# Kernel optimization log

Measured on AMD Instinct MI355X. Metric: run time of the kernel, lower is better.

## Reference

```python
import jax, jax.numpy as jnp
import numpy as np


def setup_inputs() -> dict:
    key = jax.random.key(0)
    B, L = 32, 512
    k1, k2, k3, k4 = jax.random.split(key, 4)
    acids = jax.random.normal(k1, (B, L), dtype=jnp.float32)
    mask = jnp.ones((B, L), dtype=jnp.float32)
    # Self-avoiding-style lattice walk: unit step along a random axis each move.
    axis = jax.random.randint(k3, (B, L - 1), 0, 3)
    sign = jax.random.randint(k4, (B, L - 1), 0, 2) * 2 - 1
    steps = (jax.nn.one_hot(axis, 3, dtype=jnp.int32) * sign[..., None]).astype(jnp.int32)
    idx = jnp.concatenate([jnp.zeros((B, 1, 3), jnp.int32), jnp.cumsum(steps, axis=1)], axis=1)
    idx = jnp.clip(idx, -(L - 1), L - 1)  # keep coords in the op's valid range
    return {"acids": acids, "mask": mask, "idx": idx, "protein_length": 512, "window_size": 9}


def reference(acids, mask, idx, protein_length, window_size):
    # acids: [B, L] float, mask: [B, L] float, idx: [B, L, 3] int lattice coords.
    L, W = protein_length, window_size
    B = acids.shape[0]
    W3 = W * W * W
    half = W // 2

    # Map walk coords [-(L-1), L-1] -> even grid coords [0, 4(L-1)].
    idx2 = 2 * (idx + (L - 1))                          # [B, L, 3] int32, all even
    # AVG pool window [2] stride 1 VALID on even ints -> exact integer midpoints.
    inter_idx = (idx2[:, :-1, :] + idx2[:, 1:, :]) // 2  # [B, L-1, 3] odd coords
    # 2 * avgpool(acids) + 1 == acids[i] + acids[i+1] + 1
    inter_vals = acids[:, :-1] + acids[:, 1:] + 1.0      # [B, L-1]

    cidx = jnp.concatenate([idx2, inter_idx], axis=1)    # [B, M, 3], M = 2L-1
    cval = jnp.concatenate([acids, inter_vals], axis=1)  # [B, M]
    cmask = jnp.concatenate([mask, mask[:, 1:]], axis=1) # [B, M]

    # Per residue i: a W^3 window centered at idx2[:, i]. Scatter every snake
    # point (residues + bond midpoints) that falls inside the window.
    rel = cidx[:, None, :, :] - idx2[:, :, None, :] + half     # [B, L, M, 3]
    valid = jnp.all((rel >= 0) & (rel < W), axis=-1)           # [B, L, M]
    lin = (rel[..., 0] * W + rel[..., 1]) * W + rel[..., 2]    # [B, L, M]
    lin = jnp.where(valid, lin, 0)
    val = jnp.where(valid, (cval * cmask)[:, None, :], 0.0)    # [B, L, M]

    b_off = jnp.arange(B, dtype=jnp.int32)[:, None, None] * (L * W3)
    i_off = jnp.arange(L, dtype=jnp.int32)[None, :, None] * W3
    g = (b_off + i_off + lin).reshape(-1)
    lattice = jnp.zeros((B * L * W3,), dtype=acids.dtype).at[g].add(val.reshape(-1))
    return lattice.reshape(B, L, W, W, W, 1)
```

## Files before the change

kernel.cpp:

```cpp
#include <hip/hip_runtime.h>
#include <hip/hip_bf16.h>


constexpr int L    = 512;
constexpr int W    = 9;
constexpr int W3   = W * W * W;
constexpr int HALF = W / 2;
constexpr int M    = 2 * L - 1;
constexpr int G    = 8;
constexpr int BOXW = 2 * (G - 1) + W;
constexpr int BOXN = BOXW * BOXW * BOXW;

typedef float vfloat4 __attribute__((ext_vector_type(4)));

__global__ __launch_bounds__(256) void lattice_snake_kernel(
    const float* __restrict__ acids,
    const float* __restrict__ mask,
    const int*   __restrict__ idx,
    float*       __restrict__ out)
{
    const int blk = blockIdx.x;
    const int b   = blk >> 6;
    const int g   = blk & 63;
    const int i0  = g * G;
    const int tid = threadIdx.x;

    const int*   idxb = idx   + (size_t)b * L * 3;
    const float* ab   = acids + (size_t)b * L;
    const float* mb   = mask  + (size_t)b * L;

    int cxs[G], cys[G], czs[G];
    int mnx =  1 << 30, mny =  1 << 30, mnz =  1 << 30;
    int mxx = -(1 << 30), mxy = -(1 << 30), mxz = -(1 << 30);
#pragma unroll
    for (int w = 0; w < G; ++w) {
        const int ii = i0 + w;
        const int cx = 2 * idxb[3 * ii + 0] + 2 * (L - 1);
        const int cy = 2 * idxb[3 * ii + 1] + 2 * (L - 1);
        const int cz = 2 * idxb[3 * ii + 2] + 2 * (L - 1);
        cxs[w] = cx; cys[w] = cy; czs[w] = cz;
        mnx = min(mnx, cx); mxx = max(mxx, cx);
        mny = min(mny, cy); mxy = max(mxy, cy);
        mnz = min(mnz, cz); mxz = max(mxz, cz);
    }
    const int ox = mnx - HALF, oy = mny - HALF, oz = mnz - HALF;
    const int dxd = mxx - mnx + W;
    const int dyd = mxy - mny + W;
    const int dzd = mxz - mnz + W;
    const int nbox  = dxd * dyd * dzd;
    const int dydzd = dyd * dzd;

    __shared__ float box[BOXN];
    __shared__ int   win_base[G];

    for (int k = tid; k < nbox; k += 256) box[k] = 0.0f;
    if (tid == 0) {
#pragma unroll
        for (int w = 0; w < G; ++w) {
            const int bx = cxs[w] - HALF - ox;
            const int by = cys[w] - HALF - oy;
            const int bz = czs[w] - HALF - oz;
            win_base[w] = bx * dydzd + by * dzd + bz;
        }
    }
    __syncthreads();

    for (int m = tid; m < M; m += 256) {
        int px, py, pz;
        float v;
        if (m < L) {
            px = 2 * idxb[3 * m + 0] + 2 * (L - 1);
            py = 2 * idxb[3 * m + 1] + 2 * (L - 1);
            pz = 2 * idxb[3 * m + 2] + 2 * (L - 1);
            v  = ab[m] * mb[m];
        } else {
            const int j = m - L;
            px = idxb[3 * j + 0] + idxb[3 * j + 3] + 2 * (L - 1);
            py = idxb[3 * j + 1] + idxb[3 * j + 4] + 2 * (L - 1);
            pz = idxb[3 * j + 2] + idxb[3 * j + 5] + 2 * (L - 1);
            v  = (ab[j] + ab[j + 1] + 1.0f) * mb[j + 1];
        }
        const int rx = px - ox, ry = py - oy, rz = pz - oz;
        if ((unsigned)rx < (unsigned)dxd && (unsigned)ry < (unsigned)dyd &&
            (unsigned)rz < (unsigned)dzd) {
            atomicAdd(&box[(rx * dyd + ry) * dzd + rz], v);
        }
    }
    __syncthreads();

    float* ob = out + ((size_t)b * L + i0) * W3;
    for (int e = tid * 4; e < G * W3; e += 256 * 4) {
        vfloat4 v4;
#pragma unroll
        for (int u = 0; u < 4; ++u) {
            const int ee = e + u;
            const int w  = ee / W3;
            const int k  = ee - w * W3;
            const int dx = k / 81;
            const int r  = k - dx * 81;
            const int dy = r / 9;
            const int dz = r - dy * 9;
            v4[u] = box[win_base[w] + dx * dydzd + dy * dzd + dz];
        }
        __builtin_nontemporal_store(v4, (vfloat4*)(ob + e));
    }
}

extern "C" void kernel_launch(void* const* d_in, const int* in_sizes, int n_in,
                              void* d_out, int out_size, void* d_ws, size_t ws_size,
                              hipStream_t stream) {
    const float* acids = (const float*)d_in[0];
    const float* mask  = (const float*)d_in[1];
    const int*   idx   = (const int*)d_in[2];
    float*       out   = (float*)d_out;

    const int B = in_sizes[0] / L;
    const int nblocks = B * (L / G);

    lattice_snake_kernel<<<nblocks, 256, 0, stream>>>(acids, mask, idx, out);
}
```

Measured before the change: 89.40 us.

## Halve residues per block, compute bounding box with wave shuffles

Each block now handles 4 residues instead of 8, doubling the block count and shrinking the shared box. The per-block min/max of window centers is computed in parallel with xor-shuffles instead of a serial loop in every thread. The box is zeroed with full-size vector stores, the strides are forced odd to reduce LDS bank conflicts, and launch bounds request 8 blocks per SM. The trade-off is that every block still scans all 1023 snake points, so total scan work doubles.

```diff
diff --git a/kernel.cpp b/kernel.cpp
--- a/kernel.cpp
+++ b/kernel.cpp
@@ -1,5 +1,4 @@
 #include <hip/hip_runtime.h>
-#include <hip/hip_bf16.h>
 
 
 constexpr int L    = 512;
@@ -7,21 +6,23 @@
 constexpr int W3   = W * W * W;
 constexpr int HALF = W / 2;
 constexpr int M    = 2 * L - 1;
-constexpr int G    = 8;
+constexpr int G    = 4;
+constexpr int GW3  = G * W3;
 constexpr int BOXW = 2 * (G - 1) + W;
 constexpr int BOXN = BOXW * BOXW * BOXW;
+constexpr int THREADS = 256;
 
 typedef float vfloat4 __attribute__((ext_vector_type(4)));
 
-__global__ __launch_bounds__(256) void lattice_snake_kernel(
+__global__ __launch_bounds__(THREADS, 8) void lattice_snake_kernel(
     const float* __restrict__ acids,
     const float* __restrict__ mask,
     const int*   __restrict__ idx,
     float*       __restrict__ out)
 {
     const int blk = blockIdx.x;
-    const int b   = blk >> 6;
-    const int g   = blk & 63;
+    const int b   = blk >> 7;
+    const int g   = blk & 127;
     const int i0  = g * G;
     const int tid = threadIdx.x;
 
@@ -29,43 +30,44 @@
     const float* ab   = acids + (size_t)b * L;
     const float* mb   = mask  + (size_t)b * L;
 
-    int cxs[G], cys[G], czs[G];
-    int mnx =  1 << 30, mny =  1 << 30, mnz =  1 << 30;
-    int mxx = -(1 << 30), mxy = -(1 << 30), mxz = -(1 << 30);
+    __shared__ float box[BOXN + 9];
+    __shared__ int   win_base[G];
+
+    const int w0 = tid & (G - 1);
+    const int ii = i0 + w0;
+    const int cx = 2 * idxb[3 * ii + 0] + 2 * (L - 1);
+    const int cy = 2 * idxb[3 * ii + 1] + 2 * (L - 1);
+    const int cz = 2 * idxb[3 * ii + 2] + 2 * (L - 1);
+    int mnx = cx, mxx = cx, mny = cy, mxy = cy, mnz = cz, mxz = cz;
 #pragma unroll
-    for (int w = 0; w < G; ++w) {
-        const int ii = i0 + w;
-        const int cx = 2 * idxb[3 * ii + 0] + 2 * (L - 1);
-        const int cy = 2 * idxb[3 * ii + 1] + 2 * (L - 1);
-        const int cz = 2 * idxb[3 * ii + 2] + 2 * (L - 1);
-        cxs[w] = cx; cys[w] = cy; czs[w] = cz;
-        mnx = min(mnx, cx); mxx = max(mxx, cx);
-        mny = min(mny, cy); mxy = max(mxy, cy);
-        mnz = min(mnz, cz); mxz = max(mxz, cz);
+    for (int msk = 1; msk < G; msk <<= 1) {
+        mnx = min(mnx, __shfl_xor(mnx, msk));
+        mxx = max(mxx, __shfl_xor(mxx, msk));
+        mny = min(mny, __shfl_xor(mny, msk));
+        mxy = max(mxy, __shfl_xor(mxy, msk));
+        mnz = min(mnz, __shfl_xor(mnz, msk));
+        mxz = max(mxz, __shfl_xor(mxz, msk));
     }
     const int ox = mnx - HALF, oy = mny - HALF, oz = mnz - HALF;
     const int dxd = mxx - mnx + W;
-    const int dyd = mxy - mny + W;
-    const int dzd = mxz - mnz + W;
-    const int nbox  = dxd * dyd * dzd;
+    const int dyd = (mxy - mny + W) | 1;
+    const int dzd = (mxz - mnz + W) | 1;
     const int dydzd = dyd * dzd;
 
-    __shared__ float box[BOXN];
-    __shared__ int   win_base[G];
-
-    for (int k = tid; k < nbox; k += 256) box[k] = 0.0f;
-    if (tid == 0) {
+    {
+        const vfloat4 z = {0.0f, 0.0f, 0.0f, 0.0f};
 #pragma unroll
-        for (int w = 0; w < G; ++w) {
-            const int bx = cxs[w] - HALF - ox;
-            const int by = cys[w] - HALF - oy;
-            const int bz = czs[w] - HALF - oz;
-            win_base[w] = bx * dydzd + by * dzd + bz;
-        }
+        for (int k = tid * 4; k < BOXN; k += THREADS * 4)
+            *(vfloat4*)&box[k] = z;
+    }
+    if (tid < G) {
+        win_base[tid] = (cx - HALF - ox) * dydzd +
+                        (cy - HALF - oy) * dzd +
+                        (cz - HALF - oz);
     }
     __syncthreads();
 
-    for (int m = tid; m < M; m += 256) {
+    for (int m = tid; m < M; m += THREADS) {
         int px, py, pz;
         float v;
         if (m < L) {
@@ -89,7 +91,7 @@
     __syncthreads();
 
     float* ob = out + ((size_t)b * L + i0) * W3;
-    for (int e = tid * 4; e < G * W3; e += 256 * 4) {
+    for (int e = tid * 4; e < GW3; e += THREADS * 4) {
         vfloat4 v4;
 #pragma unroll
         for (int u = 0; u < 4; ++u) {
@@ -117,5 +119,5 @@
     const int B = in_sizes[0] / L;
     const int nblocks = B * (L / G);
 
-    lattice_snake_kernel<<<nblocks, 256, 0, stream>>>(acids, mask, idx, out);
+    lattice_snake_kernel<<<nblocks, THREADS, 0, stream>>>(acids, mask, idx, out);
 }
```

After: 87.46 us. -2.2%, faster.
